# Performance work log

Hardware: AMD Instinct MI355X
Metric: run time of the kernel (lower is better)

Reference implementation:

```python
import jax, jax.numpy as jnp
import numpy as np

H = 1024
V = 50257
B = 64
T = 512


def setup_inputs() -> dict:
    key = jax.random.key(0)
    ks = jax.random.split(key, 16)
    s = 0.02
    return {
        "input_seq": jax.random.randint(ks[0], (B,), 0, V, dtype=jnp.int32),
        "last_hidden": jax.random.normal(ks[1], (1, B, H), dtype=jnp.float32),
        "encoder_outputs": jax.random.normal(ks[2], (B, T, H), dtype=jnp.float32),
        "emb": jax.random.normal(ks[3], (V, H), dtype=jnp.float32) * s,
        "W_ih": jax.random.normal(ks[4], (3 * H, H), dtype=jnp.float32) * s,
        "W_hh": jax.random.normal(ks[5], (3 * H, H), dtype=jnp.float32) * s,
        "b_ih": jnp.zeros((3 * H,), jnp.float32),
        "b_hh": jnp.zeros((3 * H,), jnp.float32),
        "W_a": jax.random.normal(ks[6], (H, H), dtype=jnp.float32) * s,
        "b_a": jnp.zeros((H,), jnp.float32),
        "W_c": jax.random.normal(ks[7], (H, 2 * H), dtype=jnp.float32) * s,
        "b_c": jnp.zeros((H,), jnp.float32),
        "W_o": jax.random.normal(ks[8], (V, H), dtype=jnp.float32) * s,
        "b_o": jnp.zeros((V,), jnp.float32),
    }


def reference(input_seq, last_hidden, encoder_outputs, emb, W_ih, W_hh, b_ih, b_hh,
              W_a, b_a, W_c, b_c, W_o, b_o):
    # Embedding lookup (dropout is identity in eval)
    x = emb[input_seq]                      # [B, H]
    h0 = last_hidden[0]                     # [B, H] (num_layers == 1)

    # Single GRU step, torch gate order (r, z, n)
    gi = x @ W_ih.T + b_ih                  # [B, 3H]
    gh = h0 @ W_hh.T + b_hh                 # [B, 3H]
    r = jax.nn.sigmoid(gi[:, :H] + gh[:, :H])
    z = jax.nn.sigmoid(gi[:, H:2 * H] + gh[:, H:2 * H])
    n = jnp.tanh(gi[:, 2 * H:] + r * gh[:, 2 * H:])
    h = (1.0 - z) * n + z * h0              # [B, H]

    # Attention, method='general': batched (replaces per-batch torch.mm loop)
    energy = jnp.einsum('bth,oh->bto', encoder_outputs, W_a) + b_a  # [B, T, H]
    scores = jnp.einsum('bh,bth->bt', h, energy)                    # [B, T]
    attn_w = jax.nn.softmax(scores, axis=1)                         # [B, T]
    context = jnp.einsum('bt,bth->bh', attn_w, encoder_outputs)     # [B, H]

    concat_input = jnp.concatenate([h, context], axis=1)            # [B, 2H]
    concat_output = jnp.tanh(concat_input @ W_c.T + b_c)            # [B, H]
    output = concat_output @ W_o.T + b_o                            # [B, V]
    hidden = h[None]                                                # [1, B, H]
    return (output, hidden)
```

## Files before the change

### kernel.cpp

```cpp
#include <hip/hip_runtime.h>
#include <hip/hip_bf16.h>
#include <cstdint>
#include <cstddef>

#define H 1024
#define V 50257
#define B 64
#define T 512

typedef __attribute__((ext_vector_type(8))) short bf16x8;
typedef __attribute__((ext_vector_type(4))) float f32x4;

__device__ __forceinline__ float sigmoidf_(float x) { return 1.0f / (1.0f + expf(-x)); }

__device__ __forceinline__ unsigned short f2bf_rn(float x) {
    __hip_bfloat16 h = __float2bfloat16(x);
    return __builtin_bit_cast(unsigned short, h);
}

__device__ __forceinline__ void gl_lds16(const float* g, float* l) {
    __builtin_amdgcn_global_load_lds(
        (const __attribute__((address_space(1))) unsigned*)g,
        (__attribute__((address_space(3))) unsigned*)l, 16, 0, 0);
}

__global__ void k_prep(const int* __restrict__ seq, const float* __restrict__ emb,
                       const float* __restrict__ h0,
                       unsigned short* __restrict__ X_bf,
                       unsigned short* __restrict__ h0_bf) {
    int i = blockIdx.x * 256 + threadIdx.x;
    int b = i >> 10, h = i & 1023;
    X_bf[i] = f2bf_rn(emb[(size_t)seq[b] * H + h]);
    h0_bf[i] = f2bf_rn(h0[i]);
}

__global__ __launch_bounds__(256) void k_mfma_bt(
    const unsigned short* __restrict__ A0, const unsigned short* __restrict__ A1, int lda,
    const float* __restrict__ B0, const float* __restrict__ B1, int ldb,
    float* __restrict__ C0, float* __restrict__ C1, int N, int KC) {
    __shared__ __align__(16) float Bs[2][128 * 64];
    const unsigned short* A = blockIdx.z ? A1 : A0;
    const float* Bm = blockIdx.z ? B1 : B0;
    float* C = (blockIdx.z ? C1 : C0) + (size_t)blockIdx.y * 64 * N;
    const int t = threadIdx.x;
    const int w = t >> 6, lane = t & 63;
    const int li = lane & 15, qu = lane >> 4;
    const int n0 = blockIdx.x * 128;
    const int k0 = blockIdx.y * KC;
    const int nsteps = KC >> 6;

    f32x4 acc[4][2];
#pragma unroll
    for (int ms = 0; ms < 4; ++ms)
#pragma unroll
        for (int nt = 0; nt < 2; ++nt) acc[ms][nt] = (f32x4){0.f, 0.f, 0.f, 0.f};

#define STG(BUF, KK)                                                            \
    {                                                                           \
        _Pragma("unroll")                                                       \
        for (int j = 0; j < 8; ++j) {                                           \
            int cidx = (w * 8 + j) * 64 + lane;                                 \
            int row = cidx >> 4, cs = cidx & 15;                                \
            int cg = cs ^ (row & 15);                                           \
            const float* gp = Bm + (size_t)(n0 + row) * ldb + (KK) + cg * 4;    \
            gl_lds16(gp, &Bs[BUF][(w * 8 + j) * 256]);                          \
        }                                                                       \
    }

    STG(0, k0)
    __syncthreads();

    for (int kt = 0; kt < nsteps; ++kt) {
        const int buf = kt & 1;
        if (kt + 1 < nsteps) STG(buf ^ 1, k0 + (kt + 1) * 64)

        const int kk = k0 + kt * 64;
#pragma unroll
        for (int ks = 0; ks < 2; ++ks) {
            bf16x8 af[4];
#pragma unroll
            for (int ms = 0; ms < 4; ++ms)
                af[ms] = *(const bf16x8*)&A[(size_t)(ms * 16 + li) * lda + kk + ks * 32 + qu * 8];
#pragma unroll
            for (int nt = 0; nt < 2; ++nt) {
                int row = w * 32 + nt * 16 + li;
                int cc0 = ks * 8 + qu * 2;
                float4 x0 = *(const float4*)&Bs[buf][row * 64 + ((cc0)     ^ (row & 15)) * 4];
                float4 x1 = *(const float4*)&Bs[buf][row * 64 + ((cc0 + 1) ^ (row & 15)) * 4];
                bf16x8 bfr;
                bfr[0] = (short)f2bf_rn(x0.x); bfr[1] = (short)f2bf_rn(x0.y);
                bfr[2] = (short)f2bf_rn(x0.z); bfr[3] = (short)f2bf_rn(x0.w);
                bfr[4] = (short)f2bf_rn(x1.x); bfr[5] = (short)f2bf_rn(x1.y);
                bfr[6] = (short)f2bf_rn(x1.z); bfr[7] = (short)f2bf_rn(x1.w);
#pragma unroll
                for (int ms = 0; ms < 4; ++ms)
                    acc[ms][nt] = __builtin_amdgcn_mfma_f32_16x16x32_bf16(
                        af[ms], bfr, acc[ms][nt], 0, 0, 0);
            }
        }
        __syncthreads();
    }
#undef STG

#pragma unroll
    for (int nt = 0; nt < 2; ++nt) {
        int col = n0 + w * 32 + nt * 16 + li;
#pragma unroll
        for (int ms = 0; ms < 4; ++ms)
#pragma unroll
            for (int j = 0; j < 4; ++j)
                C[(size_t)(ms * 16 + qu * 4 + j) * N + col] = acc[ms][nt][j];
    }
}

__global__ __launch_bounds__(256) void k_mfma_wa(const unsigned short* __restrict__ cat_bf,
                                                 const float* __restrict__ Wa,
                                                 float* __restrict__ Pu) {
    const int t = threadIdx.x;
    const int w = t >> 6, lane = t & 63;
    const int li = lane & 15, qu = lane >> 4;
    const int n0 = blockIdx.x * 128;
    const int k0 = blockIdx.y * 256;

    f32x4 acc[4][2];
#pragma unroll
    for (int ms = 0; ms < 4; ++ms)
#pragma unroll
        for (int nt = 0; nt < 2; ++nt) acc[ms][nt] = (f32x4){0.f, 0.f, 0.f, 0.f};

    for (int kt = 0; kt < 4; ++kt) {
        const int kk = k0 + kt * 64;
#pragma unroll
        for (int ks = 0; ks < 2; ++ks) {
            bf16x8 af[4];
#pragma unroll
            for (int ms = 0; ms < 4; ++ms)
                af[ms] = *(const bf16x8*)&cat_bf[(size_t)(ms * 16 + li) * 2048 + kk + ks * 32 + qu * 8];
            const int kb = kk + ks * 32 + qu * 8;
#pragma unroll
            for (int nt = 0; nt < 2; ++nt) {
                int col = n0 + w * 32 + nt * 16 + li;
                bf16x8 bfr;
#pragma unroll
                for (int e = 0; e < 8; ++e)
                    bfr[e] = (short)f2bf_rn(Wa[(size_t)(kb + e) * H + col]);
#pragma unroll
                for (int ms = 0; ms < 4; ++ms)
                    acc[ms][nt] = __builtin_amdgcn_mfma_f32_16x16x32_bf16(
                        af[ms], bfr, acc[ms][nt], 0, 0, 0);
            }
        }
    }
    float* C = Pu + (size_t)blockIdx.y * 64 * H;
#pragma unroll
    for (int nt = 0; nt < 2; ++nt) {
        int col = n0 + w * 32 + nt * 16 + li;
#pragma unroll
        for (int ms = 0; ms < 4; ++ms)
#pragma unroll
            for (int j = 0; j < 4; ++j)
                C[(size_t)(ms * 16 + qu * 4 + j) * H + col] = acc[ms][nt][j];
    }
}

__global__ void k_gru(const float* __restrict__ Pgi, const float* __restrict__ Pgh,
                      const float* __restrict__ bih, const float* __restrict__ bhh,
                      const float* __restrict__ h0, unsigned short* __restrict__ cat_bf,
                      float* __restrict__ hid) {
    int i = blockIdx.x * 256 + threadIdx.x;
    int b = i >> 10, h = i & 1023;
    float gr = bih[h], gz = bih[H + h], gn = bih[2 * H + h];
    float hr = bhh[h], hz = bhh[H + h], hn = bhh[2 * H + h];
#pragma unroll
    for (int kt = 0; kt < 4; ++kt) {
        const float* pi = Pgi + (size_t)kt * B * 3 * H + (size_t)b * 3 * H;
        const float* ph = Pgh + (size_t)kt * B * 3 * H + (size_t)b * 3 * H;
        gr += pi[h]; gz += pi[H + h]; gn += pi[2 * H + h];
        hr += ph[h]; hz += ph[H + h]; hn += ph[2 * H + h];
    }
    float r = sigmoidf_(gr + hr);
    float z = sigmoidf_(gz + hz);
    float n = tanhf(gn + r * hn);
    float hv = (1.0f - z) * n + z * h0[i];
    cat_bf[(size_t)b * 2048 + h] = f2bf_rn(hv);
    hid[i] = hv;
}

__global__ __launch_bounds__(256) void k_flash(const float* __restrict__ Pu,
                                               const float* __restrict__ enc,
                                               float* __restrict__ Pm,
                                               float* __restrict__ Pl,
                                               float* __restrict__ Pc) {
    const int g = blockIdx.x * 4 + (threadIdx.x >> 6);
    const int lane = threadIdx.x & 63;
    const int b = g >> 6, ch = g & 63;

    float4 uu[4];
#pragma unroll
    for (int it = 0; it < 4; ++it) {
        int col = (it * 64 + lane) * 4;
        float4 s = *(const float4*)&Pu[(size_t)b * H + col];
#pragma unroll
        for (int kt = 1; kt < 4; ++kt) {
            float4 p = *(const float4*)&Pu[(size_t)kt * B * H + (size_t)b * H + col];
            s.x += p.x; s.y += p.y; s.z += p.z; s.w += p.w;
        }
        uu[it] = s;
    }

    float m = -3.4e38f, l = 0.f;
    float4 c[4] = {{0,0,0,0},{0,0,0,0},{0,0,0,0},{0,0,0,0}};
    const float* ebase = enc + ((size_t)b * T + ch * 8) * H;

#pragma unroll 2
    for (int tt = 0; tt < 8; ++tt) {
        float4 e[4];
#pragma unroll
        for (int it = 0; it < 4; ++it)
            e[it] = *(const float4*)&ebase[(size_t)tt * H + (it * 64 + lane) * 4];
        float s = 0.f;
#pragma unroll
        for (int it = 0; it < 4; ++it)
            s += uu[it].x * e[it].x + uu[it].y * e[it].y +
                 uu[it].z * e[it].z + uu[it].w * e[it].w;
#pragma unroll
        for (int o = 32; o; o >>= 1) s += __shfl_xor(s, o, 64);
        float mn = fmaxf(m, s);
        float scale = __expf(m - mn);
        float p = __expf(s - mn);
        l = l * scale + p;
#pragma unroll
        for (int it = 0; it < 4; ++it) {
            c[it].x = fmaf(p, e[it].x, c[it].x * scale);
            c[it].y = fmaf(p, e[it].y, c[it].y * scale);
            c[it].z = fmaf(p, e[it].z, c[it].z * scale);
            c[it].w = fmaf(p, e[it].w, c[it].w * scale);
        }
        m = mn;
    }

    if (lane == 0) { Pm[g] = m; Pl[g] = l; }
#pragma unroll
    for (int it = 0; it < 4; ++it)
        *(float4*)&Pc[(size_t)g * H + (it * 64 + lane) * 4] = c[it];
}

__global__ void k_fcomb(const float* __restrict__ Pm, const float* __restrict__ Pl,
                        const float* __restrict__ Pc, unsigned short* __restrict__ cat_bf) {
    const int b = blockIdx.x;
    const int col = threadIdx.x * 4;
    float M = -3.4e38f;
#pragma unroll 8
    for (int i = 0; i < 64; ++i) M = fmaxf(M, Pm[b * 64 + i]);
    float L = 0.f;
    float4 cc = {0, 0, 0, 0};
#pragma unroll 4
    for (int i = 0; i < 64; ++i) {
        float wgt = __expf(Pm[b * 64 + i] - M);
        L += Pl[b * 64 + i] * wgt;
        float4 p = *(const float4*)&Pc[(size_t)(b * 64 + i) * H + col];
        cc.x += wgt * p.x; cc.y += wgt * p.y;
        cc.z += wgt * p.z; cc.w += wgt * p.w;
    }
    float inv = 1.0f / L;
    ushort4 o;
    o.x = f2bf_rn(cc.x * inv); o.y = f2bf_rn(cc.y * inv);
    o.z = f2bf_rn(cc.z * inv); o.w = f2bf_rn(cc.w * inv);
    *(ushort4*)&cat_bf[(size_t)b * 2048 + 1024 + col] = o;
}

__global__ void k_co(const float* __restrict__ Pc, const float* __restrict__ bc,
                     unsigned short* __restrict__ co_bf) {
    int i = blockIdx.x * 256 + threadIdx.x;
    int h = i & 1023;
    float s = bc[h];
#pragma unroll
    for (int kt = 0; kt < 4; ++kt) s += Pc[kt * (B * H) + i];
    co_bf[i] = f2bf_rn(tanhf(s));
}

__global__ __launch_bounds__(256) void k_out_mfma(const unsigned short* __restrict__ co_bf,
                                                  const float* __restrict__ Wo,
                                                  const float* __restrict__ bo,
                                                  float* __restrict__ out) {
    __shared__ __align__(16) float Bs[2][128 * 64];
    const int t = threadIdx.x;
    const int w = t >> 6, lane = t & 63;
    const int li = lane & 15, qu = lane >> 4;
    const int v0 = blockIdx.x * 128;

    f32x4 acc[4][2];
#pragma unroll
    for (int ms = 0; ms < 4; ++ms)
#pragma unroll
        for (int nt = 0; nt < 2; ++nt) acc[ms][nt] = (f32x4){0.f, 0.f, 0.f, 0.f};

#define STAGE(BUF, KK)                                                          \
    {                                                                           \
        _Pragma("unroll")                                                       \
        for (int j = 0; j < 8; ++j) {                                           \
            int cidx = (w * 8 + j) * 64 + lane;                                 \
            int row = cidx >> 4, cs = cidx & 15;                                \
            int cg = cs ^ (row & 15);                                           \
            int vr = v0 + row; if (vr >= V) vr = V - 1;                         \
            const float* gp = Wo + (size_t)vr * H + (KK) + cg * 4;              \
            gl_lds16(gp, &Bs[BUF][(w * 8 + j) * 256]);                          \
        }                                                                       \
    }

    STAGE(0, 0)
    __syncthreads();

    for (int kt = 0; kt < 16; ++kt) {
        const int buf = kt & 1;
        if (kt < 15) STAGE(buf ^ 1, (kt + 1) * 64)

        const int kk = kt * 64;
#pragma unroll
        for (int ks = 0; ks < 2; ++ks) {
            bf16x8 af[4];
#pragma unroll
            for (int ms = 0; ms < 4; ++ms)
                af[ms] = *(const bf16x8*)&co_bf[(size_t)(ms * 16 + li) * H + kk + ks * 32 + qu * 8];
#pragma unroll
            for (int nt = 0; nt < 2; ++nt) {
                int row = w * 32 + nt * 16 + li;
                int cc0 = ks * 8 + qu * 2;
                float4 x0 = *(const float4*)&Bs[buf][row * 64 + ((cc0)     ^ (row & 15)) * 4];
                float4 x1 = *(const float4*)&Bs[buf][row * 64 + ((cc0 + 1) ^ (row & 15)) * 4];
                bf16x8 bfr;
                bfr[0] = (short)f2bf_rn(x0.x); bfr[1] = (short)f2bf_rn(x0.y);
                bfr[2] = (short)f2bf_rn(x0.z); bfr[3] = (short)f2bf_rn(x0.w);
                bfr[4] = (short)f2bf_rn(x1.x); bfr[5] = (short)f2bf_rn(x1.y);
                bfr[6] = (short)f2bf_rn(x1.z); bfr[7] = (short)f2bf_rn(x1.w);
#pragma unroll
                for (int ms = 0; ms < 4; ++ms)
                    acc[ms][nt] = __builtin_amdgcn_mfma_f32_16x16x32_bf16(
                        af[ms], bfr, acc[ms][nt], 0, 0, 0);
            }
        }
        __syncthreads();
    }
#undef STAGE

#pragma unroll
    for (int nt = 0; nt < 2; ++nt) {
        int v = v0 + w * 32 + nt * 16 + li;
        if (v < V) {
            float bov = bo[v];
#pragma unroll
            for (int ms = 0; ms < 4; ++ms)
#pragma unroll
                for (int j = 0; j < 4; ++j)
                    out[(size_t)(ms * 16 + qu * 4 + j) * V + v] = acc[ms][nt][j] + bov;
        }
    }
}

extern "C" void kernel_launch(void* const* d_in, const int* in_sizes, int n_in,
                              void* d_out, int out_size, void* d_ws, size_t ws_size,
                              hipStream_t stream) {
    (void)in_sizes; (void)n_in; (void)out_size; (void)ws_size;
    const int*   seq = (const int*)d_in[0];
    const float* h0  = (const float*)d_in[1];
    const float* enc = (const float*)d_in[2];
    const float* emb = (const float*)d_in[3];
    const float* Wih = (const float*)d_in[4];
    const float* Whh = (const float*)d_in[5];
    const float* bih = (const float*)d_in[6];
    const float* bhh = (const float*)d_in[7];
    const float* Wa  = (const float*)d_in[8];
    const float* Wc  = (const float*)d_in[10];
    const float* bc  = (const float*)d_in[11];
    const float* Wo  = (const float*)d_in[12];
    const float* bo  = (const float*)d_in[13];

    float* out = (float*)d_out;
    float* hid = out + (size_t)B * V;

    float* ws   = (float*)d_ws;
    float* Pgi  = ws;
    float* Pgh  = Pgi + 786432;
    float* Pu   = Pgh + 786432;
    float* Pm   = Pu + 262144;
    float* Pl   = Pm + 4096;
    float* Pc   = Pl + 4096;
    float* Pcg  = Pc + 4194304;
    unsigned short* X_bf  = (unsigned short*)(Pcg + 262144);
    unsigned short* h0_bf = X_bf + 65536;
    unsigned short* cat_bf = h0_bf + 65536;
    unsigned short* co_bf  = cat_bf + 131072;

    k_prep<<<256, 256, 0, stream>>>(seq, emb, h0, X_bf, h0_bf);
    k_mfma_bt<<<dim3(24, 4, 2), 256, 0, stream>>>(X_bf, h0_bf, H, Wih, Whh, H,
                                                  Pgi, Pgh, 3 * H, 256);
    k_gru<<<256, 256, 0, stream>>>(Pgi, Pgh, bih, bhh, h0, cat_bf, hid);
    k_mfma_wa<<<dim3(8, 4), 256, 0, stream>>>(cat_bf, Wa, Pu);
    k_flash<<<1024, 256, 0, stream>>>(Pu, enc, Pm, Pl, Pc);
    k_fcomb<<<64, 256, 0, stream>>>(Pm, Pl, Pc, cat_bf);
    k_mfma_bt<<<dim3(8, 4, 1), 256, 0, stream>>>(cat_bf, cat_bf, 2 * H, Wc, Wc, 2 * H,
                                                 Pcg, Pcg, H, 512);
    k_co<<<256, 256, 0, stream>>>(Pcg, bc, co_bf);
    k_out_mfma<<<(V + 127) / 128, 256, 0, stream>>>(co_bf, Wo, bo, out);
}
```

Before: 160.6 us.

## Drop block barriers in MFMA GEMMs and merge flash partials inside each block

In the staged bf16 MFMA GEMM kernels, each wave reads back only the LDS rows it staged itself. The block-wide __syncthreads calls are therefore replaced with a per-wave `s_waitcnt vmcnt(0)` drain plus a scheduling barrier, so waves no longer wait on each other. The flash-attention kernel now combines its four waves' online-softmax partials through LDS, writing one partial per block instead of one per wave. This cuts the partial-context buffer and the work the final combine kernel does by a factor of four. It depends on the row-ownership invariant and adds an LDS barrier and extra exp work in the flash epilogue.

```diff
diff --git a/kernel.cpp b/kernel.cpp
--- a/kernel.cpp
+++ b/kernel.cpp
@@ -22,6 +22,11 @@
     __builtin_amdgcn_global_load_lds(
         (const __attribute__((address_space(1))) unsigned*)g,
         (__attribute__((address_space(3))) unsigned*)l, 16, 0, 0);
+}
+
+__device__ __forceinline__ void wave_vm_drain() {
+    asm volatile("s_waitcnt vmcnt(0)" ::: "memory");
+    __builtin_amdgcn_sched_barrier(0);
 }
 
 __global__ void k_prep(const int* __restrict__ seq, const float* __restrict__ emb,
@@ -68,10 +73,10 @@
     }
 
     STG(0, k0)
-    __syncthreads();
 
     for (int kt = 0; kt < nsteps; ++kt) {
         const int buf = kt & 1;
+        wave_vm_drain();
         if (kt + 1 < nsteps) STG(buf ^ 1, k0 + (kt + 1) * 64)
 
         const int kk = k0 + kt * 64;
@@ -98,7 +103,6 @@
                         af[ms], bfr, acc[ms][nt], 0, 0, 0);
             }
         }
-        __syncthreads();
     }
 #undef STG
 
@@ -191,9 +195,8 @@
                                                float* __restrict__ Pm,
                                                float* __restrict__ Pl,
                                                float* __restrict__ Pc) {
-    const int g = blockIdx.x * 4 + (threadIdx.x >> 6);
-    const int lane = threadIdx.x & 63;
-    const int b = g >> 6, ch = g & 63;
+    const int b = blockIdx.x >> 4, ch = blockIdx.x & 15;
+    const int w = threadIdx.x >> 6, lane = threadIdx.x & 63;
 
     float4 uu[4];
 #pragma unroll
@@ -210,7 +213,7 @@
 
     float m = -3.4e38f, l = 0.f;
     float4 c[4] = {{0,0,0,0},{0,0,0,0},{0,0,0,0},{0,0,0,0}};
-    const float* ebase = enc + ((size_t)b * T + ch * 8) * H;
+    const float* ebase = enc + ((size_t)b * T + ch * 32 + w * 8) * H;
 
 #pragma unroll 2
     for (int tt = 0; tt < 8; ++tt) {
@@ -239,10 +242,31 @@
         m = mn;
     }
 
-    if (lane == 0) { Pm[g] = m; Pl[g] = l; }
+    __shared__ float Lm[4], Ll[4];
+    __shared__ __align__(16) float Lc[4][H];
 #pragma unroll
     for (int it = 0; it < 4; ++it)
-        *(float4*)&Pc[(size_t)g * H + (it * 64 + lane) * 4] = c[it];
+        *(float4*)&Lc[w][(it * 64 + lane) * 4] = c[it];
+    if (lane == 0) { Lm[w] = m; Ll[w] = l; }
+    __syncthreads();
+
+    float M = fmaxf(fmaxf(Lm[0], Lm[1]), fmaxf(Lm[2], Lm[3]));
+    float e0 = __expf(Lm[0] - M), e1 = __expf(Lm[1] - M),
+          e2 = __expf(Lm[2] - M), e3 = __expf(Lm[3] - M);
+    float L = Ll[0] * e0 + Ll[1] * e1 + Ll[2] * e2 + Ll[3] * e3;
+    int col = threadIdx.x * 4;
+    float4 c0 = *(const float4*)&Lc[0][col];
+    float4 c1 = *(const float4*)&Lc[1][col];
+    float4 c2 = *(const float4*)&Lc[2][col];
+    float4 c3 = *(const float4*)&Lc[3][col];
+    float4 cc;
+    cc.x = c0.x * e0 + c1.x * e1 + c2.x * e2 + c3.x * e3;
+    cc.y = c0.y * e0 + c1.y * e1 + c2.y * e2 + c3.y * e3;
+    cc.z = c0.z * e0 + c1.z * e1 + c2.z * e2 + c3.z * e3;
+    cc.w = c0.w * e0 + c1.w * e1 + c2.w * e2 + c3.w * e3;
+    const int rec = blockIdx.x;
+    if (threadIdx.x == 0) { Pm[rec] = M; Pl[rec] = L; }
+    *(float4*)&Pc[(size_t)rec * H + col] = cc;
 }
 
 __global__ void k_fcomb(const float* __restrict__ Pm, const float* __restrict__ Pl,
@@ -250,15 +274,15 @@
     const int b = blockIdx.x;
     const int col = threadIdx.x * 4;
     float M = -3.4e38f;
-#pragma unroll 8
-    for (int i = 0; i < 64; ++i) M = fmaxf(M, Pm[b * 64 + i]);
+#pragma unroll
+    for (int i = 0; i < 16; ++i) M = fmaxf(M, Pm[b * 16 + i]);
     float L = 0.f;
     float4 cc = {0, 0, 0, 0};
 #pragma unroll 4
-    for (int i = 0; i < 64; ++i) {
-        float wgt = __expf(Pm[b * 64 + i] - M);
-        L += Pl[b * 64 + i] * wgt;
-        float4 p = *(const float4*)&Pc[(size_t)(b * 64 + i) * H + col];
+    for (int i = 0; i < 16; ++i) {
+        float wgt = __expf(Pm[b * 16 + i] - M);
+        L += Pl[b * 16 + i] * wgt;
+        float4 p = *(const float4*)&Pc[(size_t)(b * 16 + i) * H + col];
         cc.x += wgt * p.x; cc.y += wgt * p.y;
         cc.z += wgt * p.z; cc.w += wgt * p.w;
     }
@@ -309,10 +333,10 @@
     }
 
     STAGE(0, 0)
-    __syncthreads();
 
     for (int kt = 0; kt < 16; ++kt) {
         const int buf = kt & 1;
+        wave_vm_drain();
         if (kt < 15) STAGE(buf ^ 1, (kt + 1) * 64)
 
         const int kk = kt * 64;
@@ -339,7 +363,6 @@
                         af[ms], bfr, acc[ms][nt], 0, 0, 0);
             }
         }
-        __syncthreads();
     }
 #undef STAGE
 
@@ -383,9 +406,9 @@
     float* Pgh  = Pgi + 786432;
     float* Pu   = Pgh + 786432;
     float* Pm   = Pu + 262144;
-    float* Pl   = Pm + 4096;
-    float* Pc   = Pl + 4096;
-    float* Pcg  = Pc + 4194304;
+    float* Pl   = Pm + 1024;
+    float* Pc   = Pl + 1024;
+    float* Pcg  = Pc + 1048576;
     unsigned short* X_bf  = (unsigned short*)(Pcg + 262144);
     unsigned short* h0_bf = X_bf + 65536;
     unsigned short* cat_bf = h0_bf + 65536;
```

Result: faster. 142.4 us (-11.3%).
